# Kernel tuning notes

Measured on AMD Instinct MI355X. Metric: run time of the kernel, lower is better.

The kernel has to match this reference:

```python
import jax, jax.numpy as jnp
import numpy as np

N = 100000        # nodes
E = 3200000       # edges (avg degree 32)
NFEAT = 512
NHID = 256
NCLASS = 64
NLAYERS = 8
TAU = 0.5


def setup_inputs() -> dict:
    key = jax.random.key(0)
    ks = jax.random.split(key, 9)
    X = jax.random.normal(ks[0], (N, NFEAT), dtype=jnp.float32)
    edge_row = jax.random.randint(ks[1], (E,), 0, N, dtype=jnp.int32)
    edge_col = jax.random.randint(ks[2], (E,), 0, N, dtype=jnp.int32)
    # edge weights ~ 1/avg_degree so spmm is roughly norm-preserving (like a normalized adjacency)
    edge_w = jax.random.uniform(ks[3], (E,), dtype=jnp.float32) / 16.0
    W_init = jax.random.normal(ks[4], (NFEAT, NHID), dtype=jnp.float32) / np.sqrt(NFEAT).astype(np.float32)
    b_init = jnp.zeros((NHID,), dtype=jnp.float32)
    # original reset_parameters zeroes gamma and W; use small random values so the
    # computation is numerically non-trivial (same math either way)
    gammas = jax.random.normal(ks[5], (NLAYERS,), dtype=jnp.float32) * 0.1
    Ws = jax.random.normal(ks[6], (NLAYERS, NHID, NHID), dtype=jnp.float32) / np.sqrt(NHID).astype(np.float32)
    W_sort = jax.random.normal(ks[7], (NHID, NCLASS), dtype=jnp.float32) / np.sqrt(NHID).astype(np.float32)
    b_sort = jnp.zeros((NCLASS,), dtype=jnp.float32)
    return {"X": X, "edge_row": edge_row, "edge_col": edge_col, "edge_w": edge_w,
            "W_init": W_init, "b_init": b_init, "gammas": gammas, "Ws": Ws,
            "W_sort": W_sort, "b_sort": b_sort}


def reference(X, edge_row, edge_col, edge_w, W_init, b_init, gammas, Ws, W_sort, b_sort):
    # eval mode: F.dropout is identity
    H = X @ W_init + b_init                      # [N, NHID] init_dim_reduction
    I = jnp.eye(NHID, dtype=H.dtype)
    betas = TAU / jnp.arange(1, NLAYERS + 1, dtype=H.dtype)

    def spmm(M):
        # out[i] = sum_{e: row[e]=i} w[e] * M[col[e]]
        return jax.ops.segment_sum(edge_w[:, None] * M[edge_col], edge_row, num_segments=N)

    def step(carry, inp):
        Xc, acc = carry
        gamma, W, beta = inp
        AX = spmm(Xc)                             # sparse A @ X
        acc = acc + AX @ ((1.0 - beta) * I + beta * W)
        Xn = gamma * (Xc - AX)                    # next_x for the following layer
        return (Xn, acc), None

    (_, outputs), _ = jax.lax.scan(step, (H, H), (gammas, Ws, betas))
    return jax.nn.log_softmax(outputs @ W_sort + b_sort, axis=1)
```

## Files before the change

### kernel.cpp

```cpp
#include <hip/hip_runtime.h>

#define NNODES 100000
#define NEDGES 3200000
#define NFEAT  512
#define NHID   256
#define NCLS   64
#define NLAYERS 8
#define SCAN_NB ((NNODES + 1023) / 1024)

typedef short s8v __attribute__((ext_vector_type(8)));
typedef float f4v __attribute__((ext_vector_type(4)));

__device__ __forceinline__ float bf2f(unsigned short u) {
    union { unsigned int i; float f; } v; v.i = ((unsigned int)u) << 16; return v.f;
}
__device__ __forceinline__ unsigned short f2bf(float f) {
    union { float f; unsigned int u; } v; v.f = f;
    unsigned int u = v.u;
    u += 0x7FFFu + ((u >> 16) & 1u);
    return (unsigned short)(u >> 16);
}
__device__ __forceinline__ float ldf(const void* p, size_t i, int f32) {
    return f32 ? ((const float*)p)[i] : bf2f(((const unsigned short*)p)[i]);
}

__global__ void probe_kernel(const unsigned short* __restrict__ ew, int* __restrict__ flag) {
    int i = threadIdx.x;
    unsigned short v = ew[2 * i];
    bool bad = (v & 0x8000u) || (v > 0x3D80u);
    unsigned long long m = __ballot(bad);
    if (i == 0) *flag = (m != 0ull) ? 1 : 0;
}

__global__ void hist_kernel(const int* __restrict__ row, int* __restrict__ counts) {
    int e = blockIdx.x * 256 + threadIdx.x;
    if (e < NEDGES) atomicAdd(&counts[row[e]], 1);
}

__global__ void scan_local(const int* __restrict__ counts, int* __restrict__ row_ptr,
                           int* __restrict__ bsum) {
    __shared__ int lds[1024];
    const int tid = threadIdx.x;
    const int i = blockIdx.x * 1024 + tid;
    int v = (i < NNODES) ? counts[i] : 0;
    lds[tid] = v;
    __syncthreads();
    for (int off = 1; off < 1024; off <<= 1) {
        int t = (tid >= off) ? lds[tid - off] : 0;
        __syncthreads();
        lds[tid] += t;
        __syncthreads();
    }
    if (i < NNODES) row_ptr[i] = lds[tid] - v;
    if (tid == 1023) bsum[blockIdx.x] = lds[1023];
}

__global__ void scan_bsum(int* __restrict__ bsum) {
    if (threadIdx.x == 0) {
        int acc = 0;
        for (int i = 0; i < SCAN_NB; ++i) { int v = bsum[i]; bsum[i] = acc; acc += v; }
        bsum[SCAN_NB] = acc;
    }
}

__global__ void scan_add(int* __restrict__ row_ptr, int* __restrict__ cursor,
                         const int* __restrict__ bsum) {
    const int i = blockIdx.x * 1024 + threadIdx.x;
    if (i < NNODES) {
        int v = row_ptr[i] + bsum[blockIdx.x];
        row_ptr[i] = v;
        cursor[i]  = v;
    }
    if (i == NNODES) row_ptr[NNODES] = bsum[SCAN_NB];
}

__global__ void scatter_kernel(const int* __restrict__ row, const int* __restrict__ col,
                               const void* __restrict__ w, int* __restrict__ cursor,
                               int* __restrict__ col_s, float* __restrict__ w_s,
                               const int* __restrict__ flagp) {
    const int f32 = *flagp;
    int e = blockIdx.x * 256 + threadIdx.x;
    if (e < NEDGES) {
        int r = row[e];
        int pos = atomicAdd(&cursor[r], 1);
        col_s[pos] = col[e];
        w_s[pos]  = ldf(w, e, f32);
    }
}

template<int K, int N>
__global__ void pack_b(const void* __restrict__ src, unsigned short* __restrict__ dst,
                       const int* __restrict__ flagp) {
    const int f32 = *flagp;
    const int NT = N / 16;
    const int total = (K / 32) * NT * 64;
    int tid = blockIdx.x * 256 + threadIdx.x;
    if (tid >= total) return;
    int lane = tid & 63, rest = tid >> 6;
    int nt = rest % NT, ks = rest / NT;
    int n  = nt * 16 + (lane & 15);
    int kb = ks * 32 + (lane >> 4) * 8;
    unsigned short tmp[8];
#pragma unroll
    for (int j = 0; j < 8; ++j) tmp[j] = f2bf(ldf(src, (size_t)(kb + j) * N + n, f32));
#pragma unroll
    for (int j = 0; j < 8; ++j) dst[(size_t)tid * 8 + j] = tmp[j];
}

__global__ void pack_wcomb(const void* __restrict__ Ws, const void* __restrict__ Wsort,
                           unsigned short* __restrict__ dst, const int* __restrict__ flagp) {
    const int f32 = *flagp;
    int tid = blockIdx.x * 256 + threadIdx.x;
    if (tid >= 16384) return;
    int lane = tid & 63;
    int rest = tid >> 6;
    int nt = rest & 3;
    int ks = (rest >> 2) & 7;
    int l  = rest >> 5;
    int n  = nt * 16 + (lane & 15);
    int kb = ks * 32 + (lane >> 4) * 8;
    float beta = 0.5f / (float)(l + 1);
    float ombeta = 1.0f - beta;
    const size_t wl = (size_t)l * NHID * NHID;
    unsigned short tmp[8];
#pragma unroll
    for (int j = 0; j < 8; ++j) {
        int k = kb + j;
        float s = 0.0f;
        for (int q = 0; q < NHID; ++q)
            s = fmaf(ldf(Ws, wl + (size_t)k * NHID + q, f32),
                     ldf(Wsort, (size_t)q * NCLS + n, f32), s);
        tmp[j] = f2bf(ombeta * ldf(Wsort, (size_t)k * NCLS + n, f32) + beta * s);
    }
#pragma unroll
    for (int j = 0; j < 8; ++j) dst[(size_t)tid * 8 + j] = tmp[j];
}

template<int K, int NTT, int NTW, int MT, bool SHARE, bool ADYN, bool ACCUM, bool BIAS, bool OUTBF>
__global__ __launch_bounds__(256) void gemm_mfma(
    const void* __restrict__ Av, const s8v* __restrict__ Bp,
    const void* __restrict__ bias,
    float* __restrict__ Cf, unsigned short* __restrict__ Cb,
    const int* __restrict__ flagp)
{
    const int f32 = (ADYN || BIAS) ? *flagp : 0;
    const int N    = NTT * 16;
    const int lane = threadIdx.x & 63;
    const int wid  = threadIdx.x >> 6;
    int mbase, nt0;
    if (SHARE) {
        mbase = blockIdx.x * (MT * 16);
        nt0   = wid * NTW;
    } else {
        const int job = blockIdx.x * 4 + wid;
        mbase = job * (MT * 16);
        nt0   = 0;
    }
    if (mbase >= NNODES) return;
    const int l15  = lane & 15;
    const int quad = lane >> 4;

    f4v acc[MT][NTW];
#pragma unroll
    for (int mt = 0; mt < MT; ++mt)
#pragma unroll
        for (int nt = 0; nt < NTW; ++nt)
            acc[mt][nt] = (f4v){0.f, 0.f, 0.f, 0.f};

#pragma unroll 4
    for (int ks = 0; ks < K / 32; ++ks) {
        const int kb = ks * 32 + quad * 8;
        s8v a[MT];
        if (ADYN && f32) {
            const float* Af = (const float*)Av;
#pragma unroll
            for (int mt = 0; mt < MT; ++mt) {
                const float4* p = (const float4*)(Af + (size_t)(mbase + mt * 16 + l15) * K + kb);
                float4 x0 = p[0], x1 = p[1];
                a[mt][0] = (short)f2bf(x0.x); a[mt][1] = (short)f2bf(x0.y);
                a[mt][2] = (short)f2bf(x0.z); a[mt][3] = (short)f2bf(x0.w);
                a[mt][4] = (short)f2bf(x1.x); a[mt][5] = (short)f2bf(x1.y);
                a[mt][6] = (short)f2bf(x1.z); a[mt][7] = (short)f2bf(x1.w);
            }
        } else {
            const unsigned short* A = (const unsigned short*)Av;
#pragma unroll
            for (int mt = 0; mt < MT; ++mt)
                a[mt] = *(const s8v*)(A + (size_t)(mbase + mt * 16 + l15) * K + kb);
        }
#pragma unroll
        for (int nt = 0; nt < NTW; ++nt) {
            s8v b = Bp[(ks * NTT + nt0 + nt) * 64 + lane];
#pragma unroll
            for (int mt = 0; mt < MT; ++mt)
                acc[mt][nt] = __builtin_amdgcn_mfma_f32_16x16x32_bf16(a[mt], b, acc[mt][nt], 0, 0, 0);
        }
    }

#pragma unroll
    for (int mt = 0; mt < MT; ++mt) {
#pragma unroll
        for (int nt = 0; nt < NTW; ++nt) {
#pragma unroll
            for (int r = 0; r < 4; ++r) {
                int row = mbase + mt * 16 + quad * 4 + r;
                int col = (nt0 + nt) * 16 + l15;
                float v = acc[mt][nt][r];
                if (BIAS) v += ldf(bias, col, f32);
                size_t idx = (size_t)row * N + col;
                if (OUTBF) {
                    Cb[idx] = f2bf(v);
                } else {
                    if (ACCUM) v += Cf[idx];
                    Cf[idx] = v;
                }
            }
        }
    }
}

template<bool LAST>
__global__ __launch_bounds__(256) void spmm_kernel(
    const int* __restrict__ row_ptr, const int* __restrict__ col_s,
    const float* __restrict__ w_s, const unsigned short* __restrict__ Xc,
    unsigned short* __restrict__ AXb, unsigned short* __restrict__ Xn,
    const void* __restrict__ gammas, int layer, const int* __restrict__ flagp)
{
    const int wid  = threadIdx.x >> 6;
    const int lane = threadIdx.x & 63;
    const int node = blockIdx.x * 4 + wid;
    if (node >= NNODES) return;
    const int start = row_ptr[node];
    const int end   = row_ptr[node + 1];
    const int fo    = lane * 4;
    float a0 = 0.f, a1 = 0.f, a2 = 0.f, a3 = 0.f;
    int e = start;
    for (; e + 8 <= end; e += 8) {
        int   c[8];
        float w[8];
#pragma unroll
        for (int j = 0; j < 8; ++j) { c[j] = col_s[e + j]; w[j] = w_s[e + j]; }
        ushort4 q[8];
#pragma unroll
        for (int j = 0; j < 8; ++j)
            q[j] = *(const ushort4*)(Xc + (size_t)c[j] * NHID + fo);
#pragma unroll
        for (int j = 0; j < 8; ++j) {
            a0 = fmaf(w[j], bf2f(q[j].x), a0);
            a1 = fmaf(w[j], bf2f(q[j].y), a1);
            a2 = fmaf(w[j], bf2f(q[j].z), a2);
            a3 = fmaf(w[j], bf2f(q[j].w), a3);
        }
    }
    for (; e < end; ++e) {
        const int   c = col_s[e];
        const float w = w_s[e];
        ushort4 q = *(const ushort4*)(Xc + (size_t)c * NHID + fo);
        a0 = fmaf(w, bf2f(q.x), a0);
        a1 = fmaf(w, bf2f(q.y), a1);
        a2 = fmaf(w, bf2f(q.z), a2);
        a3 = fmaf(w, bf2f(q.w), a3);
    }
    ushort4 axo;
    axo.x = f2bf(a0); axo.y = f2bf(a1); axo.z = f2bf(a2); axo.w = f2bf(a3);
    *(ushort4*)(AXb + (size_t)node * NHID + fo) = axo;
    if (!LAST) {
        const float g = ldf(gammas, layer, *flagp);
        ushort4 xi = *(const ushort4*)(Xc + (size_t)node * NHID + fo);
        ushort4 xno;
        xno.x = f2bf(g * (bf2f(xi.x) - a0));
        xno.y = f2bf(g * (bf2f(xi.y) - a1));
        xno.z = f2bf(g * (bf2f(xi.z) - a2));
        xno.w = f2bf(g * (bf2f(xi.w) - a3));
        *(ushort4*)(Xn + (size_t)node * NHID + fo) = xno;
    }
}

__global__ __launch_bounds__(256) void lsm_kernel(const float* __restrict__ Z,
                                                  void* __restrict__ out,
                                                  const int* __restrict__ flagp) {
    const int f32 = *flagp;
    const int wid  = threadIdx.x >> 6;
    const int lane = threadIdx.x & 63;
    const int row  = blockIdx.x * 4 + wid;
    if (row >= NNODES) return;
    float z = Z[(size_t)row * NCLS + lane];
    float m = z;
#pragma unroll
    for (int off = 32; off >= 1; off >>= 1) m = fmaxf(m, __shfl_xor(m, off, 64));
    float s = __expf(z - m);
#pragma unroll
    for (int off = 32; off >= 1; off >>= 1) s += __shfl_xor(s, off, 64);
    float r = z - m - __logf(s);
    size_t idx = (size_t)row * NCLS + lane;
    if (f32) ((float*)out)[idx] = r;
    else     ((unsigned short*)out)[idx] = f2bf(r);
}

extern "C" void kernel_launch(void* const* d_in, const int* in_sizes, int n_in,
                              void* d_out, int out_size, void* d_ws, size_t ws_size,
                              hipStream_t stream)
{
    const void* X      = d_in[0];
    const int*  erow   = (const int*)d_in[1];
    const int*  ecol   = (const int*)d_in[2];
    const void* ew     = d_in[3];
    const void* Winit  = d_in[4];
    const void* binit  = d_in[5];
    const void* gammas = d_in[6];
    const void* Ws     = d_in[7];
    const void* Wsort  = d_in[8];
    const void* bsort  = d_in[9];

    char* p = (char*)d_ws;
    auto alloc = [&](size_t bytes) -> char* {
        char* r = p; p += (bytes + 255) & ~(size_t)255; return r;
    };
    int*            flag   = (int*)           alloc(256);
    float*          Zacc   = (float*)         alloc((size_t)NNODES * NCLS * 4);
    unsigned short* Xc0    = (unsigned short*)alloc((size_t)NNODES * NHID * 2);
    unsigned short* Xc1    = (unsigned short*)alloc((size_t)NNODES * NHID * 2);
    unsigned short* AXb    = (unsigned short*)alloc((size_t)NNODES * NHID * 2);
    int*            counts = (int*)           alloc((size_t)(NNODES + 1) * 4);
    int*            row_ptr= (int*)           alloc((size_t)(NNODES + 1) * 4);
    int*            cursor = (int*)           alloc((size_t)(NNODES + 1) * 4);
    int*            bsum   = (int*)           alloc((size_t)(SCAN_NB + 1) * 4);
    int*            col_s  = (int*)           alloc((size_t)NEDGES * 4);
    float*          w_s    = (float*)         alloc((size_t)NEDGES * 4);
    unsigned short* WinitP = (unsigned short*)alloc((size_t)NFEAT * NHID * 2);
    unsigned short* WsortP = (unsigned short*)alloc((size_t)NHID * NCLS * 2);
    unsigned short* WcombP = (unsigned short*)alloc((size_t)NLAYERS * NHID * NCLS * 2);

    probe_kernel<<<1, 64, 0, stream>>>((const unsigned short*)ew, flag);

    hipMemsetAsync(counts, 0, (size_t)NNODES * 4, stream);
    hist_kernel<<<NEDGES / 256, 256, 0, stream>>>(erow, counts);
    scan_local<<<SCAN_NB, 1024, 0, stream>>>(counts, row_ptr, bsum);
    scan_bsum<<<1, 64, 0, stream>>>(bsum);
    scan_add<<<SCAN_NB, 1024, 0, stream>>>(row_ptr, cursor, bsum);
    scatter_kernel<<<NEDGES / 256, 256, 0, stream>>>(erow, ecol, ew, cursor, col_s, w_s, flag);

    pack_b<NFEAT, NHID><<<64, 256, 0, stream>>>(Winit, WinitP, flag);
    pack_b<NHID, NCLS><<<8, 256, 0, stream>>>(Wsort, WsortP, flag);
    pack_wcomb<<<64, 256, 0, stream>>>(Ws, Wsort, WcombP, flag);

    gemm_mfma<NFEAT, 16, 4, 2, true, true, false, true, true>
        <<<NNODES / 32, 256, 0, stream>>>(X, (const s8v*)WinitP, binit, nullptr, Xc0, flag);

    const int g16 = (NNODES / 16 + 3) / 4;

    gemm_mfma<NHID, 4, 4, 1, false, false, false, true, false>
        <<<g16, 256, 0, stream>>>(Xc0, (const s8v*)WsortP, bsort, Zacc, nullptr, flag);

    unsigned short* cur = Xc0;
    unsigned short* nxt = Xc1;
    for (int l = 0; l < NLAYERS; ++l) {
        if (l < NLAYERS - 1)
            spmm_kernel<false><<<NNODES / 4, 256, 0, stream>>>(row_ptr, col_s, w_s, cur, AXb, nxt, gammas, l, flag);
        else
            spmm_kernel<true><<<NNODES / 4, 256, 0, stream>>>(row_ptr, col_s, w_s, cur, AXb, nxt, gammas, l, flag);
        gemm_mfma<NHID, 4, 4, 1, false, false, true, false, false>
            <<<g16, 256, 0, stream>>>(AXb, (const s8v*)WcombP + (size_t)l * 2048, nullptr, Zacc, nullptr, flag);
        unsigned short* t = cur; cur = nxt; nxt = t;
    }

    lsm_kernel<<<NNODES / 4, 256, 0, stream>>>(Zacc, d_out, flag);
}
```

Baseline: 2.927 ms.

## Fuse SpMM with per-layer projection GEMM and pack edge col/weight

Each SpMM block now handles 16 nodes, stages the AX rows (and H on layer 0) in swizzled shared memory, and runs the 256x64 combined-weight MFMA projection in the same kernel, accumulating into Zacc. This removes the AX round trip through global memory, the separate per-layer GEMM launches and the standalone Wsort GEMM. Edge column and weight are packed into one 64-bit record, so each edge costs one load instead of two. In exchange, a block now walks four node rows in sequence per wave and needs a barrier before the MFMA stage, which may reduce latency hiding in the gather.

```diff
diff --git a/kernel.cpp b/kernel.cpp
--- a/kernel.cpp
+++ b/kernel.cpp
@@ -23,6 +23,11 @@
 __device__ __forceinline__ float ldf(const void* p, size_t i, int f32) {
     return f32 ? ((const float*)p)[i] : bf2f(((const unsigned short*)p)[i]);
 }
+__device__ __forceinline__ int em_col(long long m) { return (int)(unsigned int)m; }
+__device__ __forceinline__ float em_w(long long m) {
+    union { int i; float f; } u; u.i = (int)((unsigned long long)m >> 32); return u.f;
+}
+#define SW(off, row) ((off) ^ (((row) & 7) << 4))
 
 __global__ void probe_kernel(const unsigned short* __restrict__ ew, int* __restrict__ flag) {
     int i = threadIdx.x;
@@ -76,15 +81,17 @@
 
 __global__ void scatter_kernel(const int* __restrict__ row, const int* __restrict__ col,
                                const void* __restrict__ w, int* __restrict__ cursor,
-                               int* __restrict__ col_s, float* __restrict__ w_s,
+                               long long* __restrict__ em,
                                const int* __restrict__ flagp) {
     const int f32 = *flagp;
     int e = blockIdx.x * 256 + threadIdx.x;
     if (e < NEDGES) {
         int r = row[e];
         int pos = atomicAdd(&cursor[r], 1);
-        col_s[pos] = col[e];
-        w_s[pos]  = ldf(w, e, f32);
+        float wv = ldf(w, e, f32);
+        union { float f; unsigned int u; } uw; uw.f = wv;
+        long long rec = ((long long)uw.u << 32) | (unsigned int)col[e];
+        em[pos] = rec;
     }
 }
 
@@ -219,60 +226,98 @@
     }
 }
 
-template<bool LAST>
-__global__ __launch_bounds__(256) void spmm_kernel(
-    const int* __restrict__ row_ptr, const int* __restrict__ col_s,
-    const float* __restrict__ w_s, const unsigned short* __restrict__ Xc,
-    unsigned short* __restrict__ AXb, unsigned short* __restrict__ Xn,
+template<bool FIRST, bool LAST>
+__global__ __launch_bounds__(256) void spmm_fused(
+    const int* __restrict__ row_ptr, const long long* __restrict__ em,
+    const unsigned short* __restrict__ Xc, unsigned short* __restrict__ Xn,
+    const s8v* __restrict__ WcombL, const s8v* __restrict__ WsortP,
+    const void* __restrict__ bsort, float* __restrict__ Zacc,
     const void* __restrict__ gammas, int layer, const int* __restrict__ flagp)
 {
+    __shared__ unsigned short axl[16 * 256];
+    __shared__ unsigned short hxl[FIRST ? 16 * 256 : 4];
     const int wid  = threadIdx.x >> 6;
     const int lane = threadIdx.x & 63;
-    const int node = blockIdx.x * 4 + wid;
-    if (node >= NNODES) return;
-    const int start = row_ptr[node];
-    const int end   = row_ptr[node + 1];
-    const int fo    = lane * 4;
-    float a0 = 0.f, a1 = 0.f, a2 = 0.f, a3 = 0.f;
-    int e = start;
-    for (; e + 8 <= end; e += 8) {
-        int   c[8];
-        float w[8];
-#pragma unroll
-        for (int j = 0; j < 8; ++j) { c[j] = col_s[e + j]; w[j] = w_s[e + j]; }
-        ushort4 q[8];
-#pragma unroll
-        for (int j = 0; j < 8; ++j)
-            q[j] = *(const ushort4*)(Xc + (size_t)c[j] * NHID + fo);
-#pragma unroll
-        for (int j = 0; j < 8; ++j) {
-            a0 = fmaf(w[j], bf2f(q[j].x), a0);
-            a1 = fmaf(w[j], bf2f(q[j].y), a1);
-            a2 = fmaf(w[j], bf2f(q[j].z), a2);
-            a3 = fmaf(w[j], bf2f(q[j].w), a3);
-        }
-    }
-    for (; e < end; ++e) {
-        const int   c = col_s[e];
-        const float w = w_s[e];
-        ushort4 q = *(const ushort4*)(Xc + (size_t)c * NHID + fo);
-        a0 = fmaf(w, bf2f(q.x), a0);
-        a1 = fmaf(w, bf2f(q.y), a1);
-        a2 = fmaf(w, bf2f(q.z), a2);
-        a3 = fmaf(w, bf2f(q.w), a3);
-    }
-    ushort4 axo;
-    axo.x = f2bf(a0); axo.y = f2bf(a1); axo.z = f2bf(a2); axo.w = f2bf(a3);
-    *(ushort4*)(AXb + (size_t)node * NHID + fo) = axo;
-    if (!LAST) {
-        const float g = ldf(gammas, layer, *flagp);
-        ushort4 xi = *(const ushort4*)(Xc + (size_t)node * NHID + fo);
-        ushort4 xno;
-        xno.x = f2bf(g * (bf2f(xi.x) - a0));
-        xno.y = f2bf(g * (bf2f(xi.y) - a1));
-        xno.z = f2bf(g * (bf2f(xi.z) - a2));
-        xno.w = f2bf(g * (bf2f(xi.w) - a3));
-        *(ushort4*)(Xn + (size_t)node * NHID + fo) = xno;
+    const int mbase = blockIdx.x * 16;
+    const int fo = lane * 4;
+    const int f32 = *flagp;
+    const float g = LAST ? 0.f : ldf(gammas, layer, f32);
+
+    for (int s = 0; s < 4; ++s) {
+        const int row  = wid * 4 + s;
+        const int node = mbase + row;
+        const int start = row_ptr[node];
+        const int end   = row_ptr[node + 1];
+        float a0 = 0.f, a1 = 0.f, a2 = 0.f, a3 = 0.f;
+        int e = start;
+        for (; e + 8 <= end; e += 8) {
+            long long m[8];
+#pragma unroll
+            for (int j = 0; j < 8; ++j) m[j] = em[e + j];
+            ushort4 q[8];
+#pragma unroll
+            for (int j = 0; j < 8; ++j)
+                q[j] = *(const ushort4*)(Xc + (size_t)em_col(m[j]) * NHID + fo);
+#pragma unroll
+            for (int j = 0; j < 8; ++j) {
+                float w = em_w(m[j]);
+                a0 = fmaf(w, bf2f(q[j].x), a0);
+                a1 = fmaf(w, bf2f(q[j].y), a1);
+                a2 = fmaf(w, bf2f(q[j].z), a2);
+                a3 = fmaf(w, bf2f(q[j].w), a3);
+            }
+        }
+        for (; e < end; ++e) {
+            long long m = em[e];
+            float w = em_w(m);
+            ushort4 q = *(const ushort4*)(Xc + (size_t)em_col(m) * NHID + fo);
+            a0 = fmaf(w, bf2f(q.x), a0);
+            a1 = fmaf(w, bf2f(q.y), a1);
+            a2 = fmaf(w, bf2f(q.z), a2);
+            a3 = fmaf(w, bf2f(q.w), a3);
+        }
+        ushort4 axo;
+        axo.x = f2bf(a0); axo.y = f2bf(a1); axo.z = f2bf(a2); axo.w = f2bf(a3);
+        *(ushort4*)((char*)axl + SW(row * 512 + lane * 8, row)) = axo;
+        if (FIRST || !LAST) {
+            ushort4 xi = *(const ushort4*)(Xc + (size_t)node * NHID + fo);
+            if constexpr (FIRST)
+                *(ushort4*)((char*)hxl + SW(row * 512 + lane * 8, row)) = xi;
+            if constexpr (!LAST) {
+                ushort4 xno;
+                xno.x = f2bf(g * (bf2f(xi.x) - a0));
+                xno.y = f2bf(g * (bf2f(xi.y) - a1));
+                xno.z = f2bf(g * (bf2f(xi.z) - a2));
+                xno.w = f2bf(g * (bf2f(xi.w) - a3));
+                *(ushort4*)(Xn + (size_t)node * NHID + fo) = xno;
+            }
+        }
+    }
+    __syncthreads();
+
+    const int l15  = lane & 15;
+    const int quad = lane >> 4;
+    f4v acc = (f4v){0.f, 0.f, 0.f, 0.f};
+#pragma unroll
+    for (int ks = 0; ks < NHID / 32; ++ks) {
+        const int boff = SW(l15 * 512 + ks * 64 + quad * 16, l15);
+        s8v a = *(const s8v*)((const char*)axl + boff);
+        s8v b = WcombL[(ks * 4 + wid) * 64 + lane];
+        acc = __builtin_amdgcn_mfma_f32_16x16x32_bf16(a, b, acc, 0, 0, 0);
+        if constexpr (FIRST) {
+            s8v h  = *(const s8v*)((const char*)hxl + boff);
+            s8v b2 = WsortP[(ks * 4 + wid) * 64 + lane];
+            acc = __builtin_amdgcn_mfma_f32_16x16x32_bf16(h, b2, acc, 0, 0, 0);
+        }
+    }
+#pragma unroll
+    for (int r = 0; r < 4; ++r) {
+        const int row = mbase + quad * 4 + r;
+        const int col = wid * 16 + l15;
+        const size_t idx = (size_t)row * NCLS + col;
+        float v = acc[r];
+        if constexpr (FIRST) Zacc[idx] = v + ldf(bsort, col, f32);
+        else                 Zacc[idx] += v;
     }
 }
 
@@ -320,13 +365,11 @@
     float*          Zacc   = (float*)         alloc((size_t)NNODES * NCLS * 4);
     unsigned short* Xc0    = (unsigned short*)alloc((size_t)NNODES * NHID * 2);
     unsigned short* Xc1    = (unsigned short*)alloc((size_t)NNODES * NHID * 2);
-    unsigned short* AXb    = (unsigned short*)alloc((size_t)NNODES * NHID * 2);
     int*            counts = (int*)           alloc((size_t)(NNODES + 1) * 4);
     int*            row_ptr= (int*)           alloc((size_t)(NNODES + 1) * 4);
     int*            cursor = (int*)           alloc((size_t)(NNODES + 1) * 4);
     int*            bsum   = (int*)           alloc((size_t)(SCAN_NB + 1) * 4);
-    int*            col_s  = (int*)           alloc((size_t)NEDGES * 4);
-    float*          w_s    = (float*)         alloc((size_t)NEDGES * 4);
+    long long*      em     = (long long*)     alloc((size_t)NEDGES * 8);
     unsigned short* WinitP = (unsigned short*)alloc((size_t)NFEAT * NHID * 2);
     unsigned short* WsortP = (unsigned short*)alloc((size_t)NHID * NCLS * 2);
     unsigned short* WcombP = (unsigned short*)alloc((size_t)NLAYERS * NHID * NCLS * 2);
@@ -338,7 +381,7 @@
     scan_local<<<SCAN_NB, 1024, 0, stream>>>(counts, row_ptr, bsum);
     scan_bsum<<<1, 64, 0, stream>>>(bsum);
     scan_add<<<SCAN_NB, 1024, 0, stream>>>(row_ptr, cursor, bsum);
-    scatter_kernel<<<NEDGES / 256, 256, 0, stream>>>(erow, ecol, ew, cursor, col_s, w_s, flag);
+    scatter_kernel<<<NEDGES / 256, 256, 0, stream>>>(erow, ecol, ew, cursor, em, flag);
 
     pack_b<NFEAT, NHID><<<64, 256, 0, stream>>>(Winit, WinitP, flag);
     pack_b<NHID, NCLS><<<8, 256, 0, stream>>>(Wsort, WsortP, flag);
@@ -347,20 +390,20 @@
     gemm_mfma<NFEAT, 16, 4, 2, true, true, false, true, true>
         <<<NNODES / 32, 256, 0, stream>>>(X, (const s8v*)WinitP, binit, nullptr, Xc0, flag);
 
-    const int g16 = (NNODES / 16 + 3) / 4;
-
-    gemm_mfma<NHID, 4, 4, 1, false, false, false, true, false>
-        <<<g16, 256, 0, stream>>>(Xc0, (const s8v*)WsortP, bsort, Zacc, nullptr, flag);
-
     unsigned short* cur = Xc0;
     unsigned short* nxt = Xc1;
+    const int fgrid = NNODES / 16;
     for (int l = 0; l < NLAYERS; ++l) {
-        if (l < NLAYERS - 1)
-            spmm_kernel<false><<<NNODES / 4, 256, 0, stream>>>(row_ptr, col_s, w_s, cur, AXb, nxt, gammas, l, flag);
+        const s8v* Wl = (const s8v*)WcombP + (size_t)l * 2048;
+        if (l == 0)
+            spmm_fused<true, false><<<fgrid, 256, 0, stream>>>(
+                row_ptr, em, cur, nxt, Wl, (const s8v*)WsortP, bsort, Zacc, gammas, l, flag);
+        else if (l < NLAYERS - 1)
+            spmm_fused<false, false><<<fgrid, 256, 0, stream>>>(
+                row_ptr, em, cur, nxt, Wl, (const s8v*)WsortP, bsort, Zacc, gammas, l, flag);
         else
-            spmm_kernel<true><<<NNODES / 4, 256, 0, stream>>>(row_ptr, col_s, w_s, cur, AXb, nxt, gammas, l, flag);
-        gemm_mfma<NHID, 4, 4, 1, false, false, true, false, false>
-            <<<g16, 256, 0, stream>>>(AXb, (const s8v*)WcombP + (size_t)l * 2048, nullptr, Zacc, nullptr, flag);
+            spmm_fused<false, true><<<fgrid, 256, 0, stream>>>(
+                row_ptr, em, cur, nxt, Wl, (const s8v*)WsortP, bsort, Zacc, gammas, l, flag);
         unsigned short* t = cur; cur = nxt; nxt = t;
     }
 
```

After: 2.877 ms. No clear change (-1.7%).
